# Optimization experiments

Hardware: AMD Instinct MI355X
Metric: run time of the kernel (lower is better)

## Reference

```python
import jax, jax.numpy as jnp
import numpy as np

NUM_USERS, NUM_ITEMS, NUM_GROUPS = 100000, 50000, 20000
D = 64
B, M = 16384, 50


def setup_inputs() -> dict:
    key = jax.random.key(0)
    ks = jax.random.split(key, 16)
    inp = {
        "group_inputs": jax.random.randint(ks[0], (B,), 0, NUM_GROUPS),
        "item_inputs": jax.random.randint(ks[1], (B,), 0, NUM_ITEMS),
        "member_ids": jax.random.randint(ks[2], (B, M), 0, NUM_USERS),
        "member_lengths": jax.random.randint(ks[3], (B,), 0, M),
        # embedding tables (xavier-ish scale)
        "user_table": jax.random.normal(ks[4], (NUM_USERS, D), jnp.float32) * 0.05,
        "item_table": jax.random.normal(ks[5], (NUM_ITEMS, D), jnp.float32) * 0.05,
        "group_table": jax.random.normal(ks[6], (NUM_GROUPS, D), jnp.float32) * 0.05,
        # attention MLP: 2D -> 16 -> 1
        "att_w1": jax.random.normal(ks[7], (2 * D, 16), jnp.float32) * 0.1,
        "att_b1": jnp.zeros((16,), jnp.float32),
        "att_w2": jax.random.normal(ks[8], (16, 1), jnp.float32) * 0.1,
        "att_b2": jnp.zeros((1,), jnp.float32),
        # predict MLP: 3D -> 8 -> 1
        "pred_w1": jax.random.normal(ks[9], (3 * D, 8), jnp.float32) * 0.1,
        "pred_b1": jnp.zeros((8,), jnp.float32),
        "pred_w2": jax.random.normal(ks[10], (8, 1), jnp.float32) * 0.1,
        "pred_b2": jnp.zeros((1,), jnp.float32),
    }
    return inp


def reference(group_inputs, item_inputs, member_ids, member_lengths,
              user_table, item_table, group_table,
              att_w1, att_b1, att_w2, att_b2,
              pred_w1, pred_b1, pred_w2, pred_b2):
    # mask: at least one valid member per group
    mask = jnp.arange(M)[None, :] <= member_lengths[:, None]          # [B, M] bool
    mem_e = user_table[member_ids]                                    # [B, M, D]
    item_e = item_table[item_inputs]                                  # [B, D]

    # attention over members: concat(member, item) -> 16 -> 1
    gi = jnp.concatenate(
        [mem_e, jnp.broadcast_to(item_e[:, None, :], mem_e.shape)], axis=-1)  # [B, M, 2D]
    h = jax.nn.relu(jnp.einsum('bmk,kh->bmh', gi, att_w1) + att_b1)   # [B, M, 16]
    scores = (jnp.einsum('bmh,ho->bmo', h, att_w2) + att_b2)[..., 0]  # [B, M]
    scores = jnp.where(mask, scores, -jnp.inf)
    at_wt = jax.nn.softmax(scores, axis=-1)                           # [B, M]

    g_att = jnp.einsum('bm,bmd->bd', at_wt, mem_e)                    # [B, D]
    g = g_att + group_table[group_inputs]                             # [B, D]

    elem = g * item_e
    new_e = jnp.concatenate([elem, g, item_e], axis=-1)               # [B, 3D]
    ph = jax.nn.relu(new_e @ pred_w1 + pred_b1)                       # [B, 8]
    y = jax.nn.sigmoid(ph @ pred_w2 + pred_b2)                        # [B, 1]
    return y
```

## Files before the change

### kernel.cpp

```cpp
#include <hip/hip_runtime.h>
#include <math.h>

constexpr int MM = 50;
constexpr int DD = 64;
constexpr int HH = 16;
constexpr int PH = 8;
constexpr int WAVES_PER_BLOCK = 4;
constexpr int SLOTS  = 56;

__device__ __forceinline__ unsigned bf16rne(float f) {
    const unsigned u = __float_as_uint(f);
    return (u + 0x7FFFu + ((u >> 16) & 1u)) >> 16;
}

__global__ __launch_bounds__(256) void precompute_kernel(
    const float* __restrict__ user_table,
    const float* __restrict__ item_table,
    const int*   __restrict__ item_inputs,
    const float* __restrict__ att_w1,
    const float* __restrict__ att_b1,
    unsigned short* __restrict__ Ubf,
    float* __restrict__ Ib,
    int nU, int B, int userBlocks)
{
    const bool isU = (int)blockIdx.x < userBlocks;
    const float4* rp;
    const float*  w1;
    float acc[HH];
    int row = 0;

    if (isU) {
        row = (int)blockIdx.x * 256 + (int)threadIdx.x;
        if (row >= nU) return;
        rp  = (const float4*)(user_table + (size_t)row * DD);
        w1  = att_w1;
        #pragma unroll
        for (int j = 0; j < HH; ++j) acc[j] = 0.0f;
    } else {
        row = ((int)blockIdx.x - userBlocks) * 256 + (int)threadIdx.x;
        if (row >= B) return;
        const int item = item_inputs[row];
        rp  = (const float4*)(item_table + (size_t)item * DD);
        w1  = att_w1 + (size_t)DD * HH;
        #pragma unroll
        for (int j = 0; j < HH; ++j) acc[j] = att_b1[j];
    }

    #pragma unroll 4
    for (int d4 = 0; d4 < DD / 4; ++d4) {
        const float4 x = rp[d4];
        const float* w = w1 + (size_t)(d4 * 4) * HH;
        #pragma unroll
        for (int j = 0; j < HH; ++j) {
            acc[j] = fmaf(x.x, w[0 * HH + j], acc[j]);
            acc[j] = fmaf(x.y, w[1 * HH + j], acc[j]);
            acc[j] = fmaf(x.z, w[2 * HH + j], acc[j]);
            acc[j] = fmaf(x.w, w[3 * HH + j], acc[j]);
        }
    }

    if (isU) {
        unsigned uw[8];
        #pragma unroll
        for (int w = 0; w < 8; ++w)
            uw[w] = bf16rne(acc[2 * w]) | (bf16rne(acc[2 * w + 1]) << 16);
        uint4* u4 = (uint4*)(Ubf + (size_t)row * HH);
        u4[0] = make_uint4(uw[0], uw[1], uw[2], uw[3]);
        u4[1] = make_uint4(uw[4], uw[5], uw[6], uw[7]);
    } else {
        float4* o4 = (float4*)(Ib + (size_t)row * HH);
        o4[0] = make_float4(acc[0],  acc[1],  acc[2],  acc[3]);
        o4[1] = make_float4(acc[4],  acc[5],  acc[6],  acc[7]);
        o4[2] = make_float4(acc[8],  acc[9],  acc[10], acc[11]);
        o4[3] = make_float4(acc[12], acc[13], acc[14], acc[15]);
    }
}

__global__ __launch_bounds__(256) void agree_main(
    const int* __restrict__ group_inputs,
    const int* __restrict__ item_inputs,
    const int* __restrict__ member_ids,
    const int* __restrict__ member_lengths,
    const float* __restrict__ user_table,
    const float* __restrict__ item_table,
    const float* __restrict__ group_table,
    const float* __restrict__ att_w2,
    const float* __restrict__ att_b2,
    const float* __restrict__ pred_w1,
    const float* __restrict__ pred_b1,
    const float* __restrict__ pred_w2,
    const float* __restrict__ pred_b2,
    const unsigned short* __restrict__ Ubf,
    const float* __restrict__ Ib,
    float* __restrict__ out,
    int B)
{
    __shared__ float2 pairs[WAVES_PER_BLOCK][SLOTS];
    __shared__ float  gbuf[WAVES_PER_BLOCK][DD];

    const int lane = threadIdx.x & 63;
    const int wv   = threadIdx.x >> 6;
    const int b    = blockIdx.x * WAVES_PER_BLOCK + wv;
    if (b >= B) return;

    const int my_m  = (lane < MM) ? lane : (MM - 1);
    const int my_id = member_ids[b * MM + my_m];
    const int len      = member_lengths[b];
    const int item_idx = item_inputs[b];
    const int gid      = group_inputs[b];

    const float item_d = item_table[(unsigned)(item_idx * DD + lane)];
    const float grp_d  = group_table[(unsigned)(gid * DD + lane)];

    const uint4* up = (const uint4*)(Ubf + ((size_t)(unsigned)my_id * HH));
    const uint4 ua = up[0], ubw = up[1];
    const float* ib = Ib + (size_t)b * HH;

    float score = att_b2[0];
    {
        const unsigned uw[8] = { ua.x, ua.y, ua.z, ua.w,
                                 ubw.x, ubw.y, ubw.z, ubw.w };
        #pragma unroll
        for (int w = 0; w < 8; ++w) {
            const float f0 = __uint_as_float(uw[w] << 16);
            const float f1 = __uint_as_float(uw[w] & 0xFFFF0000u);
            score = fmaf(fmaxf(f0 + ib[2 * w],     0.0f), att_w2[2 * w],     score);
            score = fmaf(fmaxf(f1 + ib[2 * w + 1], 0.0f), att_w2[2 * w + 1], score);
        }
    }

    const bool valid = (lane < MM) && (lane <= len);
    score = valid ? score : -INFINITY;

    float mx = score;
    #pragma unroll
    for (int off = 32; off > 0; off >>= 1) mx = fmaxf(mx, __shfl_xor(mx, off, 64));
    const float e = valid ? __expf(score - mx) : 0.0f;
    float sum = e;
    #pragma unroll
    for (int off = 32; off > 0; off >>= 1) sum += __shfl_xor(sum, off, 64);
    const float wnorm = e / sum;

    if (lane < SLOTS) pairs[wv][lane] = make_float2(wnorm, __int_as_float(my_id));
    __builtin_amdgcn_s_waitcnt(0);

    const int i = lane >> 3;
    const int j = lane & 7;

    const int mcnt   = (len < MM - 1 ? len : MM - 1) + 1;
    const int chunks = (mcnt + 7) >> 3;

    float gp[8];
    #pragma unroll
    for (int r = 0; r < 8; ++r) gp[r] = 0.0f;

    #pragma unroll 2
    for (int c = 0; c < chunks; ++c) {
        const float2 pr = pairs[wv][c * 8 + i];
        const float4* rp =
            (const float4*)(user_table
                + (size_t)(unsigned)__float_as_int(pr.y) * DD + (j << 3));
        const float4 a = rp[0];
        const float4 d = rp[1];
        const float w = pr.x;
        gp[0] = fmaf(w, a.x, gp[0]);  gp[1] = fmaf(w, a.y, gp[1]);
        gp[2] = fmaf(w, a.z, gp[2]);  gp[3] = fmaf(w, a.w, gp[3]);
        gp[4] = fmaf(w, d.x, gp[4]);  gp[5] = fmaf(w, d.y, gp[5]);
        gp[6] = fmaf(w, d.z, gp[6]);  gp[7] = fmaf(w, d.w, gp[7]);
    }

    #pragma unroll
    for (int off = 8; off < 64; off <<= 1) {
        #pragma unroll
        for (int r = 0; r < 8; ++r) gp[r] += __shfl_xor(gp[r], off, 64);
    }

    if (lane < 8) {
        float4* g4 = (float4*)&gbuf[wv][lane * 8];
        g4[0] = make_float4(gp[0], gp[1], gp[2], gp[3]);
        g4[1] = make_float4(gp[4], gp[5], gp[6], gp[7]);
    }
    __builtin_amdgcn_s_waitcnt(0);

    const float g = gbuf[wv][lane] + grp_d;

    const float elem = g * item_d;
    float p[PH];
    {
        const float* pa = pred_w1 + (size_t)lane * PH;
        const float* pb = pred_w1 + (size_t)(DD + lane) * PH;
        const float* pc = pred_w1 + (size_t)(2 * DD + lane) * PH;
        #pragma unroll
        for (int jj = 0; jj < PH; ++jj)
            p[jj] = fmaf(elem, pa[jj], fmaf(g, pb[jj], item_d * pc[jj]));
    }
    #pragma unroll
    for (int off = 32; off > 0; off >>= 1) {
        #pragma unroll
        for (int jj = 0; jj < PH; ++jj) p[jj] += __shfl_xor(p[jj], off, 64);
    }

    if (lane == 0) {
        float acc = pred_b2[0];
        #pragma unroll
        for (int jj = 0; jj < PH; ++jj)
            acc = fmaf(fmaxf(p[jj] + pred_b1[jj], 0.0f), pred_w2[jj], acc);
        out[b] = 1.0f / (1.0f + __expf(-acc));
    }
}

__global__ __launch_bounds__(256) void agree_fallback(
    const int* __restrict__ group_inputs,
    const int* __restrict__ item_inputs,
    const int* __restrict__ member_ids,
    const int* __restrict__ member_lengths,
    const float* __restrict__ user_table,
    const float* __restrict__ item_table,
    const float* __restrict__ group_table,
    const float* __restrict__ att_w1,
    const float* __restrict__ att_b1,
    const float* __restrict__ att_w2,
    const float* __restrict__ att_b2,
    const float* __restrict__ pred_w1,
    const float* __restrict__ pred_b1,
    const float* __restrict__ pred_w2,
    const float* __restrict__ pred_b2,
    float* __restrict__ out,
    int B)
{
    __shared__ float lds_wt[4][MM];
    __shared__ int   lds_id[4][MM];

    const int lane = threadIdx.x & 63;
    const int wave = threadIdx.x >> 6;
    const int b = blockIdx.x * 4 + wave;
    if (b >= B) return;

    const int my_m = (lane < MM) ? lane : (MM - 1);
    const int my_id = member_ids[b * MM + my_m];
    if (lane < MM) lds_id[wave][lane] = my_id;

    const int item_idx = item_inputs[b];
    const float item_d = item_table[(size_t)item_idx * DD + lane];

    float h[HH];
    {
        const float* w1row = att_w1 + (size_t)(DD + lane) * HH;
        #pragma unroll
        for (int j = 0; j < HH; ++j) h[j] = item_d * w1row[j];
        #pragma unroll
        for (int off = 32; off > 0; off >>= 1) {
            #pragma unroll
            for (int j = 0; j < HH; ++j) h[j] += __shfl_xor(h[j], off, 64);
        }
        #pragma unroll
        for (int j = 0; j < HH; ++j) h[j] += att_b1[j];
    }

    const float* myrow = user_table + (size_t)my_id * DD;
    #pragma unroll 4
    for (int d4 = 0; d4 < DD / 4; ++d4) {
        const float4 x = ((const float4*)myrow)[d4];
        const float* w1d = att_w1 + (size_t)(d4 * 4) * HH;
        #pragma unroll
        for (int j = 0; j < HH; ++j) {
            h[j] = fmaf(x.x, w1d[0 * HH + j], h[j]);
            h[j] = fmaf(x.y, w1d[1 * HH + j], h[j]);
            h[j] = fmaf(x.z, w1d[2 * HH + j], h[j]);
            h[j] = fmaf(x.w, w1d[3 * HH + j], h[j]);
        }
    }

    float score = att_b2[0];
    #pragma unroll
    for (int j = 0; j < HH; ++j) score = fmaf(fmaxf(h[j], 0.0f), att_w2[j], score);

    const int len = member_lengths[b];
    const bool valid = (lane < MM) && (lane <= len);
    score = valid ? score : -INFINITY;

    float mx = score;
    #pragma unroll
    for (int off = 32; off > 0; off >>= 1) mx = fmaxf(mx, __shfl_xor(mx, off, 64));
    float e = valid ? __expf(score - mx) : 0.0f;
    float sum = e;
    #pragma unroll
    for (int off = 32; off > 0; off >>= 1) sum += __shfl_xor(sum, off, 64);
    if (lane < MM) lds_wt[wave][lane] = e / sum;
    __builtin_amdgcn_s_waitcnt(0);

    const int mcnt = (len < MM - 1 ? len : MM - 1) + 1;
    float g = 0.0f;
    #pragma unroll 2
    for (int m = 0; m < mcnt; ++m) {
        g = fmaf(lds_wt[wave][m],
                 user_table[(size_t)lds_id[wave][m] * DD + lane], g);
    }
    const int gid = group_inputs[b];
    g += group_table[(size_t)gid * DD + lane];

    const float elem = g * item_d;
    float p[PH];
    {
        const float* pa = pred_w1 + (size_t)lane * PH;
        const float* pb = pred_w1 + (size_t)(DD + lane) * PH;
        const float* pc = pred_w1 + (size_t)(2 * DD + lane) * PH;
        #pragma unroll
        for (int j = 0; j < PH; ++j)
            p[j] = fmaf(elem, pa[j], fmaf(g, pb[j], item_d * pc[j]));
    }
    #pragma unroll
    for (int off = 32; off > 0; off >>= 1) {
        #pragma unroll
        for (int j = 0; j < PH; ++j) p[j] += __shfl_xor(p[j], off, 64);
    }

    if (lane == 0) {
        float acc = pred_b2[0];
        #pragma unroll
        for (int j = 0; j < PH; ++j)
            acc = fmaf(fmaxf(p[j] + pred_b1[j], 0.0f), pred_w2[j], acc);
        out[b] = 1.0f / (1.0f + __expf(-acc));
    }
}

extern "C" void kernel_launch(void* const* d_in, const int* in_sizes, int n_in,
                              void* d_out, int out_size, void* d_ws, size_t ws_size,
                              hipStream_t stream) {
    const int*   group_inputs   = (const int*)d_in[0];
    const int*   item_inputs    = (const int*)d_in[1];
    const int*   member_ids     = (const int*)d_in[2];
    const int*   member_lengths = (const int*)d_in[3];
    const float* user_table     = (const float*)d_in[4];
    const float* item_table     = (const float*)d_in[5];
    const float* group_table    = (const float*)d_in[6];
    const float* att_w1         = (const float*)d_in[7];
    const float* att_b1         = (const float*)d_in[8];
    const float* att_w2         = (const float*)d_in[9];
    const float* att_b2         = (const float*)d_in[10];
    const float* pred_w1        = (const float*)d_in[11];
    const float* pred_b1        = (const float*)d_in[12];
    const float* pred_w2        = (const float*)d_in[13];
    const float* pred_b2        = (const float*)d_in[14];
    float* out = (float*)d_out;

    const int B  = in_sizes[0];
    const int nU = in_sizes[4] / DD;
    const size_t need = (size_t)nU * HH * sizeof(unsigned short)
                      + (size_t)B  * HH * sizeof(float);
    const int blocks = (B + WAVES_PER_BLOCK - 1) / WAVES_PER_BLOCK;

    if (ws_size >= need) {
        unsigned short* Ubf = (unsigned short*)d_ws;
        float* Ib = (float*)(Ubf + (size_t)nU * HH);
        const int userBlocks = (nU + 255) / 256;
        const int itemBlocks = (B + 255) / 256;
        precompute_kernel<<<userBlocks + itemBlocks, 256, 0, stream>>>(
            user_table, item_table, item_inputs, att_w1, att_b1,
            Ubf, Ib, nU, B, userBlocks);
        agree_main<<<blocks, 256, 0, stream>>>(
            group_inputs, item_inputs, member_ids, member_lengths,
            user_table, item_table, group_table,
            att_w2, att_b2, pred_w1, pred_b1, pred_w2, pred_b2,
            Ubf, Ib, out, B);
    } else {
        agree_fallback<<<blocks, 256, 0, stream>>>(
            group_inputs, item_inputs, member_ids, member_lengths,
            user_table, item_table, group_table,
            att_w1, att_b1, att_w2, att_b2,
            pred_w1, pred_b1, pred_w2, pred_b2,
            out, B);
    }
}
```

Measured before the change: 144.8 us.

## Store fp16 user-table copy and hoist member row gathers before softmax

The precompute kernel now also writes a half-precision copy of the full user table, and stores the attention pre-activations as fp16 instead of bf16. The main kernel gathers member rows from the fp16 copy, halving gather bytes, and issues all gathers up front via register shuffles rather than LDS pairs, so they overlap the score and softmax work. The precompute pass now writes an extra 12.8 MB table each call, adds fp16 rounding error to the weighted sum, and holds more registers for the prefetched rows.

```diff
diff --git a/kernel.cpp b/kernel.cpp
--- a/kernel.cpp
+++ b/kernel.cpp
@@ -5,13 +5,9 @@
 constexpr int DD = 64;
 constexpr int HH = 16;
 constexpr int PH = 8;
-constexpr int WAVES_PER_BLOCK = 4;
-constexpr int SLOTS  = 56;
-
-__device__ __forceinline__ unsigned bf16rne(float f) {
-    const unsigned u = __float_as_uint(f);
-    return (u + 0x7FFFu + ((u >> 16) & 1u)) >> 16;
-}
+constexpr int WPB = 4;
+
+typedef _Float16 half8_t __attribute__((ext_vector_type(8)));
 
 __global__ __launch_bounds__(256) void precompute_kernel(
     const float* __restrict__ user_table,
@@ -19,8 +15,9 @@
     const int*   __restrict__ item_inputs,
     const float* __restrict__ att_w1,
     const float* __restrict__ att_b1,
-    unsigned short* __restrict__ Ubf,
-    float* __restrict__ Ib,
+    _Float16* __restrict__ Uh,
+    _Float16* __restrict__ Us,
+    float*    __restrict__ Ib,
     int nU, int B, int userBlocks)
 {
     const bool isU = (int)blockIdx.x < userBlocks;
@@ -46,7 +43,9 @@
         for (int j = 0; j < HH; ++j) acc[j] = att_b1[j];
     }
 
-    #pragma unroll 4
+    half8_t hrow[8];
+
+    #pragma unroll
     for (int d4 = 0; d4 < DD / 4; ++d4) {
         const float4 x = rp[d4];
         const float* w = w1 + (size_t)(d4 * 4) * HH;
@@ -57,16 +56,23 @@
             acc[j] = fmaf(x.z, w[2 * HH + j], acc[j]);
             acc[j] = fmaf(x.w, w[3 * HH + j], acc[j]);
         }
+        const int hw = d4 >> 1, he = (d4 & 1) * 4;
+        hrow[hw][he + 0] = (_Float16)x.x;
+        hrow[hw][he + 1] = (_Float16)x.y;
+        hrow[hw][he + 2] = (_Float16)x.z;
+        hrow[hw][he + 3] = (_Float16)x.w;
     }
 
     if (isU) {
-        unsigned uw[8];
         #pragma unroll
         for (int w = 0; w < 8; ++w)
-            uw[w] = bf16rne(acc[2 * w]) | (bf16rne(acc[2 * w + 1]) << 16);
-        uint4* u4 = (uint4*)(Ubf + (size_t)row * HH);
-        u4[0] = make_uint4(uw[0], uw[1], uw[2], uw[3]);
-        u4[1] = make_uint4(uw[4], uw[5], uw[6], uw[7]);
+            *(half8_t*)(Uh + (size_t)row * DD + w * 8) = hrow[w];
+        half8_t s0, s1;
+        #pragma unroll
+        for (int j = 0; j < 8; ++j) { s0[j] = (_Float16)acc[j];
+                                      s1[j] = (_Float16)acc[8 + j]; }
+        *(half8_t*)(Us + (size_t)row * HH)     = s0;
+        *(half8_t*)(Us + (size_t)row * HH + 8) = s1;
     } else {
         float4* o4 = (float4*)(Ib + (size_t)row * HH);
         o4[0] = make_float4(acc[0],  acc[1],  acc[2],  acc[3]);
@@ -81,7 +87,6 @@
     const int* __restrict__ item_inputs,
     const int* __restrict__ member_ids,
     const int* __restrict__ member_lengths,
-    const float* __restrict__ user_table,
     const float* __restrict__ item_table,
     const float* __restrict__ group_table,
     const float* __restrict__ att_w2,
@@ -90,17 +95,17 @@
     const float* __restrict__ pred_b1,
     const float* __restrict__ pred_w2,
     const float* __restrict__ pred_b2,
-    const unsigned short* __restrict__ Ubf,
+    const _Float16* __restrict__ Uh,
+    const _Float16* __restrict__ Us,
     const float* __restrict__ Ib,
     float* __restrict__ out,
     int B)
 {
-    __shared__ float2 pairs[WAVES_PER_BLOCK][SLOTS];
-    __shared__ float  gbuf[WAVES_PER_BLOCK][DD];
+    __shared__ float gbuf[WPB][DD];
 
     const int lane = threadIdx.x & 63;
     const int wv   = threadIdx.x >> 6;
-    const int b    = blockIdx.x * WAVES_PER_BLOCK + wv;
+    const int b    = blockIdx.x * WPB + wv;
     if (b >= B) return;
 
     const int my_m  = (lane < MM) ? lane : (MM - 1);
@@ -112,22 +117,31 @@
     const float item_d = item_table[(unsigned)(item_idx * DD + lane)];
     const float grp_d  = group_table[(unsigned)(gid * DD + lane)];
 
-    const uint4* up = (const uint4*)(Ubf + ((size_t)(unsigned)my_id * HH));
-    const uint4 ua = up[0], ubw = up[1];
+    const int mcnt = (len < MM - 1 ? len : MM - 1) + 1;
+    const int gch  = (mcnt + 7) >> 3;
+    const int i    = lane >> 3;
+    const int j    = lane & 7;
+
+    const half8_t ua = *(const half8_t*)(Us + (size_t)(unsigned)my_id * HH);
+    const half8_t ub = *(const half8_t*)(Us + (size_t)(unsigned)my_id * HH + 8);
+
+    half8_t r8[7];
+    #pragma unroll
+    for (int c = 0; c < 7; ++c) {
+        if (c < gch) {
+            const int id = __shfl(my_id, c * 8 + i, 64);
+            r8[c] = *(const half8_t*)(Uh + (size_t)(unsigned)id * DD + j * 8);
+        }
+    }
+
     const float* ib = Ib + (size_t)b * HH;
-
     float score = att_b2[0];
-    {
-        const unsigned uw[8] = { ua.x, ua.y, ua.z, ua.w,
-                                 ubw.x, ubw.y, ubw.z, ubw.w };
-        #pragma unroll
-        for (int w = 0; w < 8; ++w) {
-            const float f0 = __uint_as_float(uw[w] << 16);
-            const float f1 = __uint_as_float(uw[w] & 0xFFFF0000u);
-            score = fmaf(fmaxf(f0 + ib[2 * w],     0.0f), att_w2[2 * w],     score);
-            score = fmaf(fmaxf(f1 + ib[2 * w + 1], 0.0f), att_w2[2 * w + 1], score);
-        }
-    }
+    #pragma unroll
+    for (int k = 0; k < 8; ++k)
+        score = fmaf(fmaxf((float)ua[k] + ib[k], 0.0f), att_w2[k], score);
+    #pragma unroll
+    for (int k = 0; k < 8; ++k)
+        score = fmaf(fmaxf((float)ub[k] + ib[8 + k], 0.0f), att_w2[8 + k], score);
 
     const bool valid = (lane < MM) && (lane <= len);
     score = valid ? score : -INFINITY;
@@ -141,47 +155,28 @@
     for (int off = 32; off > 0; off >>= 1) sum += __shfl_xor(sum, off, 64);
     const float wnorm = e / sum;
 
-    if (lane < SLOTS) pairs[wv][lane] = make_float2(wnorm, __int_as_float(my_id));
-    __builtin_amdgcn_s_waitcnt(0);
-
-    const int i = lane >> 3;
-    const int j = lane & 7;
-
-    const int mcnt   = (len < MM - 1 ? len : MM - 1) + 1;
-    const int chunks = (mcnt + 7) >> 3;
-
-    float gp[8];
-    #pragma unroll
-    for (int r = 0; r < 8; ++r) gp[r] = 0.0f;
-
-    #pragma unroll 2
-    for (int c = 0; c < chunks; ++c) {
-        const float2 pr = pairs[wv][c * 8 + i];
-        const float4* rp =
-            (const float4*)(user_table
-                + (size_t)(unsigned)__float_as_int(pr.y) * DD + (j << 3));
-        const float4 a = rp[0];
-        const float4 d = rp[1];
-        const float w = pr.x;
-        gp[0] = fmaf(w, a.x, gp[0]);  gp[1] = fmaf(w, a.y, gp[1]);
-        gp[2] = fmaf(w, a.z, gp[2]);  gp[3] = fmaf(w, a.w, gp[3]);
-        gp[4] = fmaf(w, d.x, gp[4]);  gp[5] = fmaf(w, d.y, gp[5]);
-        gp[6] = fmaf(w, d.z, gp[6]);  gp[7] = fmaf(w, d.w, gp[7]);
-    }
-
+    float part[8];
+    #pragma unroll
+    for (int r = 0; r < 8; ++r) part[r] = 0.0f;
+    #pragma unroll
+    for (int c = 0; c < 7; ++c) {
+        if (c < gch) {
+            const float w = __shfl(wnorm, c * 8 + i, 64);
+            #pragma unroll
+            for (int r = 0; r < 8; ++r)
+                part[r] = fmaf(w, (float)r8[c][r], part[r]);
+        }
+    }
     #pragma unroll
     for (int off = 8; off < 64; off <<= 1) {
         #pragma unroll
-        for (int r = 0; r < 8; ++r) gp[r] += __shfl_xor(gp[r], off, 64);
-    }
-
+        for (int r = 0; r < 8; ++r) part[r] += __shfl_xor(part[r], off, 64);
+    }
     if (lane < 8) {
         float4* g4 = (float4*)&gbuf[wv][lane * 8];
-        g4[0] = make_float4(gp[0], gp[1], gp[2], gp[3]);
-        g4[1] = make_float4(gp[4], gp[5], gp[6], gp[7]);
-    }
-    __builtin_amdgcn_s_waitcnt(0);
-
+        g4[0] = make_float4(part[0], part[1], part[2], part[3]);
+        g4[1] = make_float4(part[4], part[5], part[6], part[7]);
+    }
     const float g = gbuf[wv][lane] + grp_d;
 
     const float elem = g * item_d;
@@ -346,23 +341,25 @@
 
     const int B  = in_sizes[0];
     const int nU = in_sizes[4] / DD;
-    const size_t need = (size_t)nU * HH * sizeof(unsigned short)
-                      + (size_t)B  * HH * sizeof(float);
-    const int blocks = (B + WAVES_PER_BLOCK - 1) / WAVES_PER_BLOCK;
+    const int blocks = (B + WPB - 1) / WPB;
+
+    const size_t need = (size_t)nU * (DD + HH) * sizeof(_Float16)
+                      + (size_t)B * HH * sizeof(float);
 
     if (ws_size >= need) {
-        unsigned short* Ubf = (unsigned short*)d_ws;
-        float* Ib = (float*)(Ubf + (size_t)nU * HH);
+        _Float16* Uh = (_Float16*)d_ws;
+        _Float16* Us = Uh + (size_t)nU * DD;
+        float*    Ib = (float*)(Us + (size_t)nU * HH);
         const int userBlocks = (nU + 255) / 256;
         const int itemBlocks = (B + 255) / 256;
         precompute_kernel<<<userBlocks + itemBlocks, 256, 0, stream>>>(
             user_table, item_table, item_inputs, att_w1, att_b1,
-            Ubf, Ib, nU, B, userBlocks);
+            Uh, Us, Ib, nU, B, userBlocks);
         agree_main<<<blocks, 256, 0, stream>>>(
             group_inputs, item_inputs, member_ids, member_lengths,
-            user_table, item_table, group_table,
+            item_table, group_table,
             att_w2, att_b2, pred_w1, pred_b1, pred_w2, pred_b2,
-            Ubf, Ib, out, B);
+            Uh, Us, Ib, out, B);
     } else {
         agree_fallback<<<blocks, 256, 0, stream>>>(
             group_inputs, item_inputs, member_ids, member_lengths,
```

After: 147.1 us. Within noise of the previous version (+1.6%).
